# Kernel optimization log

Hardware: AMD Instinct MI355X
Metric: run time of the kernel (lower is better)

The kernel has to match this reference:

```python
import jax, jax.numpy as jnp
import numpy as np

REG_LAMBDA = 1e-4
NEG_SLOPE = 0.2
EPS = 1e-12


def _aggregate(edge_row, edge_col, edge_val, user_emb, item_emb, W_gcn, b_gcn, W_bi, b_bi):
    num_users = user_emb.shape[0]
    N = num_users + item_emb.shape[0]
    ego = jnp.concatenate([user_emb, item_emb], axis=0)  # [N, D]
    all_embs = [ego]
    n_layers = W_gcn.shape[0]
    for l in range(n_layers):
        # sparse adjacency spmm: side = A @ ego
        side = jax.ops.segment_sum(edge_val[:, None] * ego[edge_col], edge_row, num_segments=N)
        sum_e = side @ W_gcn[l] + b_gcn[l]
        bi_e = (ego * side) @ W_bi[l] + b_bi[l]
        ego = jax.nn.leaky_relu(sum_e + bi_e, negative_slope=NEG_SLOPE)
        # mess_dropout disabled (eval-mode); L2-normalize rows
        norm = jnp.maximum(jnp.linalg.norm(ego, axis=1, keepdims=True), EPS)
        all_embs.append(ego / norm)
    final = jnp.concatenate(all_embs, axis=1)  # [N, (L+1)*D]
    return final[:num_users], final[num_users:]


def reference(user, positive, negative, edge_row, edge_col, edge_val,
              user_emb, item_emb, W_gcn, b_gcn, W_bi, b_bi):
    users_all, items_all = _aggregate(edge_row, edge_col, edge_val,
                                      user_emb, item_emb, W_gcn, b_gcn, W_bi, b_bi)
    u = users_all[user]
    p = items_all[positive]
    n = items_all[negative]
    pos_score = jnp.sum(u * p, axis=1)
    neg_score = jnp.sum(u * n, axis=1)
    # BPR: -mean(log sigmoid(pos - neg)) == mean(softplus(neg - pos))
    bpr_loss = jnp.mean(jax.nn.softplus(neg_score - pos_score))
    ego_pos = item_emb[positive]
    ego_neg = item_emb[negative]
    B = user.shape[0]
    reg_loss = REG_LAMBDA * 0.5 * (jnp.sum(ego_pos ** 2) + jnp.sum(ego_neg ** 2)) / B
    return jnp.stack([bpr_loss, reg_loss])


def setup_inputs() -> dict:
    key = jax.random.key(0)
    ks = jax.random.split(key, 12)
    U, I, D, L, NNZ, B = 50000, 100000, 128, 3, 4800000, 4096
    N = U + I
    xav = (6.0 / (D + D)) ** 0.5
    return {
        "user": jax.random.randint(ks[0], (B,), 0, U, dtype=jnp.int32),
        "positive": jax.random.randint(ks[1], (B,), 0, I, dtype=jnp.int32),
        "negative": jax.random.randint(ks[2], (B,), 0, I, dtype=jnp.int32),
        "edge_row": jax.random.randint(ks[3], (NNZ,), 0, N, dtype=jnp.int32),
        "edge_col": jax.random.randint(ks[4], (NNZ,), 0, N, dtype=jnp.int32),
        "edge_val": jax.random.uniform(ks[5], (NNZ,), dtype=jnp.float32) / 32.0,
        "user_emb": jax.random.normal(ks[6], (U, D), dtype=jnp.float32) * 0.1,
        "item_emb": jax.random.normal(ks[7], (I, D), dtype=jnp.float32) * 0.1,
        "W_gcn": jax.random.uniform(ks[8], (L, D, D), minval=-xav, maxval=xav, dtype=jnp.float32),
        "b_gcn": jax.random.uniform(ks[9], (L, D), minval=-xav, maxval=xav, dtype=jnp.float32),
        "W_bi": jax.random.uniform(ks[10], (L, D, D), minval=-xav, maxval=xav, dtype=jnp.float32),
        "b_bi": jax.random.uniform(ks[11], (L, D), minval=-xav, maxval=xav, dtype=jnp.float32),
    }
```

## Files before the change

kernel.cpp:

```cpp
#include <hip/hip_runtime.h>
#include <math.h>

#define D 128
#define NEG_SLOPE 0.2f
#define REG_LAMBDA 1e-4f
#define NORM_EPS 1e-12f

#define RPB 256
#define RPB_SHIFT 8
#define MAXB 1024
#define CHUNK 4096
#define TCSH 14
#define KEYMAX 4096

#define XPAD 264

using bf16x8 = __attribute__((ext_vector_type(8))) short;
using f32x4  = __attribute__((ext_vector_type(4))) float;
using f32x2  = __attribute__((ext_vector_type(2))) float;

__device__ __forceinline__ float wave_red(float v){
  #pragma unroll
  for (int o = 32; o > 0; o >>= 1) v += __shfl_xor(v, o, 64);
  return v;
}

__device__ __forceinline__ unsigned short f2bf(float f){
  unsigned int u = __float_as_uint(f);
  unsigned int r = (u + 0x7fffu + ((u >> 16) & 1u)) >> 16;
  return (unsigned short)r;
}
__device__ __forceinline__ float bf_lo(unsigned int x){ return __uint_as_float(x << 16); }
__device__ __forceinline__ float bf_hi(unsigned int x){ return __uint_as_float(x & 0xffff0000u); }

__global__ __launch_bounds__(256) void toq_kernel(const float* __restrict__ src, unsigned int* __restrict__ dstb,
                                                  unsigned short* __restrict__ dst8, int npairs){
  int i = blockIdx.x*256 + threadIdx.x;
  if (i >= npairs) return;
  float2 v = ((const float2*)src)[i];
  dstb[i] = (unsigned int)f2bf(v.x) | ((unsigned int)f2bf(v.y) << 16);
  int p = __builtin_amdgcn_cvt_pk_fp8_f32(v.x, v.y, 0, false);
  dst8[i] = (unsigned short)(p & 0xffff);
}

__global__ __launch_bounds__(256) void wconv_kernel(const float* __restrict__ Wg, const float* __restrict__ Wb,
                                                    unsigned short* __restrict__ Wf, int L){
  int idx = blockIdx.x*256 + threadIdx.x;
  int total = L * 256 * D;
  if (idx >= total) return;
  int l = idx >> 15;
  int rem = idx & 32767;
  int k = rem >> 7;
  int n = rem & 127;
  float v = (k < 128) ? Wg[((size_t)l*128 + k)*D + n] : Wb[((size_t)l*128 + (k-128))*D + n];
  int ks = k >> 5, quad = (k >> 3) & 3, j = k & 7;
  int t = n >> 4, ln = (quad << 4) | (n & 15);
  Wf[(size_t)l*32768 + (((ks*8 + t)*64 + ln)*8 + j)] = f2bf(v);
}

__global__ __launch_bounds__(256) void bhist_kernel(const int* __restrict__ erow, int* __restrict__ bcnt, int nnz, int nbk){
  __shared__ int h[MAXB];
  for (int i = threadIdx.x; i < nbk; i += 256) h[i] = 0;
  __syncthreads();
  int stride = gridDim.x * 256;
  for (int e = blockIdx.x*256 + threadIdx.x; e < nnz; e += stride)
    atomicAdd(&h[erow[e] >> RPB_SHIFT], 1);
  __syncthreads();
  for (int i = threadIdx.x; i < nbk; i += 256){
    int c = h[i];
    if (c) atomicAdd(&bcnt[i], c);
  }
}

__global__ __launch_bounds__(1024) void bscan_kernel(const int* __restrict__ bcnt, int* __restrict__ bbase,
                                                     int* __restrict__ bcur, int* __restrict__ rowptr,
                                                     int nbk, int nnz, int n){
  __shared__ int tmp[1024];
  int t = threadIdx.x;
  int v = (t < nbk) ? bcnt[t] : 0;
  tmp[t] = v; __syncthreads();
  #pragma unroll
  for (int off = 1; off < 1024; off <<= 1){
    int a = (t >= off) ? tmp[t-off] : 0; __syncthreads();
    tmp[t] += a; __syncthreads();
  }
  if (t < nbk){ int b = tmp[t] - v; bbase[t] = b; bcur[t] = b; }
  if (t == 0){ bbase[nbk] = nnz; rowptr[n] = nnz; }
}

__global__ __launch_bounds__(256) void bscatter_kernel(const int* __restrict__ erow, const int* __restrict__ ecol,
                                                       const float* __restrict__ eval, int* __restrict__ bcur,
                                                       int2* __restrict__ ebuf, int nnz, int nbk){
  __shared__ int2 ls[CHUNK];
  __shared__ int gdst[CHUNK];
  __shared__ int h[MAXB];
  __shared__ int hx[MAXB];
  __shared__ int tmp[256];
  int tid = threadIdx.x;
  int base = blockIdx.x * CHUNK;
  int cn = min(CHUNK, nnz - base);
  for (int i = tid; i < nbk; i += 256) h[i] = 0;
  __syncthreads();
  for (int i = tid; i < cn; i += 256)
    atomicAdd(&h[erow[base+i] >> RPB_SHIFT], 1);
  __syncthreads();
  int b0 = tid*4;
  int c0=0,c1=0,c2=0,c3=0;
  if (b0 < nbk){
    c0 = h[b0];
    if (b0+1 < nbk) c1 = h[b0+1];
    if (b0+2 < nbk) c2 = h[b0+2];
    if (b0+3 < nbk) c3 = h[b0+3];
  }
  int tsum = c0+c1+c2+c3;
  tmp[tid] = tsum; __syncthreads();
  #pragma unroll
  for (int off = 1; off < 256; off <<= 1){
    int a = (tid >= off) ? tmp[tid-off] : 0; __syncthreads();
    tmp[tid] += a; __syncthreads();
  }
  int tbase = tmp[tid] - tsum;
  if (b0 < nbk){
    hx[b0] = tbase;
    if (b0+1 < nbk) hx[b0+1] = tbase + c0;
    if (b0+2 < nbk) hx[b0+2] = tbase + c0 + c1;
    if (b0+3 < nbk) hx[b0+3] = tbase + c0 + c1 + c2;
  }
  __syncthreads();
  for (int i = tid; i < nbk; i += 256){
    int c = h[i];
    if (c > 0){
      int gb = atomicAdd(&bcur[i], c);
      h[i] = gb - hx[i];
    }
  }
  __syncthreads();
  for (int i = tid; i < cn; i += 256){
    int r = erow[base+i];
    int b = r >> RPB_SHIFT;
    int x = ecol[base+i] | ((r & (RPB-1)) << 20);
    int lpos = atomicAdd(&hx[b], 1);
    ls[lpos] = make_int2(x, __float_as_int(eval[base+i]));
    gdst[lpos] = h[b] + lpos;
  }
  __syncthreads();
  for (int i = tid; i < cn; i += 256)
    ebuf[gdst[i]] = ls[i];
}

__global__ __launch_bounds__(256) void fscatter_kernel(const int2* __restrict__ ebuf, const int* __restrict__ bbase,
                                                       int2* __restrict__ ep, int* __restrict__ rowptr,
                                                       int Tc, int n){
  __shared__ int h[KEYMAX];
  __shared__ int tsum[256];
  int b = blockIdx.x;
  int tid = threadIdx.x;
  int s = bbase[b], e = bbase[b+1];
  int row0 = b << RPB_SHIFT;
  int nk = 256 * Tc;
  for (int i = tid; i < nk; i += 256) h[i] = 0;
  __syncthreads();
  for (int i = s + tid; i < e; i += 256){
    int x = ebuf[i].x;
    int key = ((x >> 20) & 255) * Tc + ((x & 0xFFFFF) >> TCSH);
    atomicAdd(&h[key], 1);
  }
  __syncthreads();
  int my0 = tid * Tc;
  int run = 0;
  for (int j = 0; j < Tc; j++){
    int c = h[my0 + j]; h[my0 + j] = run; run += c;
  }
  tsum[tid] = run; __syncthreads();
  #pragma unroll
  for (int off = 1; off < 256; off <<= 1){
    int a = (tid >= off) ? tsum[tid-off] : 0; __syncthreads();
    tsum[tid] += a; __syncthreads();
  }
  int bt = tsum[tid] - run;
  for (int j = 0; j < Tc; j++) h[my0 + j] += bt;
  __syncthreads();
  if (row0 + tid < n) rowptr[row0 + tid] = s + h[my0];
  __syncthreads();
  for (int i = s + tid; i < e; i += 256){
    int2 E = ebuf[i];
    int x = E.x;
    int col = x & 0xFFFFF;
    int key = ((x >> 20) & 255) * Tc + (col >> TCSH);
    int p = atomicAdd(&h[key], 1);
    ep[s + p] = make_int2(col << 7, E.y);
  }
}

__global__ __launch_bounds__(256) void spmm_kernel(const int* __restrict__ rowptr, const int2* __restrict__ ep,
                                                   const unsigned char* __restrict__ egof8,
                                                   unsigned int* __restrict__ sideb, int n){
  int w = (blockIdx.x*256 + threadIdx.x) >> 6;
  int lane = threadIdx.x & 63;
  if (w >= n) return;
  int s = rowptr[w], e = rowptr[w+1];
  int sub  = lane >> 4;
  int half = lane & 15;
  float acc[8];
  #pragma unroll
  for (int j = 0; j < 8; j++) acc[j] = 0.f;
  for (int base = s; base < e; base += 16){
    int2 E[4]; uint2 X[4];
    #pragma unroll
    for (int k = 0; k < 4; k++){
      int idx = base + 4*k + sub;
      idx = idx < e ? idx : e - 1;
      E[k] = ep[idx];
    }
    #pragma unroll
    for (int k = 0; k < 4; k++)
      X[k] = *(const uint2*)(egof8 + (size_t)(unsigned)E[k].x + half*8);
    #pragma unroll
    for (int k = 0; k < 4; k++){
      float v = (base + 4*k + sub < e) ? __int_as_float(E[k].y) : 0.f;
      f32x2 d0 = __builtin_amdgcn_cvt_pk_f32_fp8((int)X[k].x, false);
      f32x2 d1 = __builtin_amdgcn_cvt_pk_f32_fp8((int)X[k].x, true);
      f32x2 d2 = __builtin_amdgcn_cvt_pk_f32_fp8((int)X[k].y, false);
      f32x2 d3 = __builtin_amdgcn_cvt_pk_f32_fp8((int)X[k].y, true);
      acc[0] = fmaf(v, d0[0], acc[0]); acc[1] = fmaf(v, d0[1], acc[1]);
      acc[2] = fmaf(v, d1[0], acc[2]); acc[3] = fmaf(v, d1[1], acc[3]);
      acc[4] = fmaf(v, d2[0], acc[4]); acc[5] = fmaf(v, d2[1], acc[5]);
      acc[6] = fmaf(v, d3[0], acc[6]); acc[7] = fmaf(v, d3[1], acc[7]);
    }
  }
  #pragma unroll
  for (int j = 0; j < 8; j++){
    acc[j] += __shfl_xor(acc[j], 16, 64);
    acc[j] += __shfl_xor(acc[j], 32, 64);
  }
  if (lane < 16){
    unsigned int o0 = (unsigned int)f2bf(acc[0]) | ((unsigned int)f2bf(acc[1]) << 16);
    unsigned int o1 = (unsigned int)f2bf(acc[2]) | ((unsigned int)f2bf(acc[3]) << 16);
    unsigned int o2 = (unsigned int)f2bf(acc[4]) | ((unsigned int)f2bf(acc[5]) << 16);
    unsigned int o3 = (unsigned int)f2bf(acc[6]) | ((unsigned int)f2bf(acc[7]) << 16);
    *(uint4*)(sideb + (size_t)w*64 + half*4) = make_uint4(o0, o1, o2, o3);
  }
}

__global__ __launch_bounds__(256, 4) void transform_kernel(const unsigned int* __restrict__ sideb,
                                                           unsigned int* __restrict__ egob,
                                                           unsigned char* __restrict__ egof8,
                                                           const unsigned short* __restrict__ Wf,
                                                           const float* __restrict__ b1, const float* __restrict__ b2,
                                                           int n){
  __shared__ __align__(16) unsigned short X[64 * XPAD];
  int row0 = blockIdx.x * 64;
  int tid = threadIdx.x;
  for (int idx = tid; idx < 64*64; idx += 256){
    int r = idx >> 6, cp = idx & 63;
    int row = row0 + r;
    unsigned int sv = 0, pv = 0;
    if (row < n){
      unsigned int s2 = sideb[(size_t)row*64 + cp];
      unsigned int eb = egob[(size_t)row*64 + cp];
      sv = s2;
      pv = (unsigned int)f2bf(bf_lo(s2) * bf_lo(eb)) | ((unsigned int)f2bf(bf_hi(s2) * bf_hi(eb)) << 16);
    }
    *(unsigned int*)&X[r*XPAD + 2*cp]       = sv;
    *(unsigned int*)&X[r*XPAD + 128 + 2*cp] = pv;
  }
  __syncthreads();

  int wave = tid >> 6, lane = tid & 63;
  int wr0 = wave * 16;
  int m = lane & 15, quad = lane >> 4;

  f32x4 acc[8];
  #pragma unroll
  for (int t = 0; t < 8; t++) acc[t] = (f32x4){0.f, 0.f, 0.f, 0.f};

  const unsigned short* arow = &X[(wr0 + m)*XPAD + quad*8];
  #pragma unroll
  for (int ks = 0; ks < 8; ks++){
    bf16x8 a = *(const bf16x8*)(arow + ks*32);
    #pragma unroll
    for (int t = 0; t < 8; t++){
      bf16x8 b = *(const bf16x8*)&Wf[((ks*8 + t)*64 + lane)*8];
      acc[t] = __builtin_amdgcn_mfma_f32_16x16x32_bf16(a, b, acc[t], 0, 0, 0);
    }
  }

  unsigned short* ego16 = (unsigned short*)egob;
  #pragma unroll
  for (int t = 0; t < 8; t++){
    int col = t*16 + m;
    float bb = b1[col] + b2[col];
    #pragma unroll
    for (int r = 0; r < 4; r++){
      int row = row0 + wr0 + quad*4 + r;
      if (row < n){
        float v = acc[t][r] + bb;
        v = v > 0.f ? v : NEG_SLOPE*v;
        ego16[(size_t)row*D + col] = f2bf(v);
        egof8[(size_t)row*D + col] =
            (unsigned char)(__builtin_amdgcn_cvt_pk_fp8_f32(v, v, 0, false) & 0xff);
      }
    }
  }
}

__global__ __launch_bounds__(256) void score_kernel(const unsigned int* __restrict__ egob, const int* __restrict__ user,
                                                    const int* __restrict__ pos, const int* __restrict__ neg,
                                                    float* __restrict__ pacc, float* __restrict__ nacc,
                                                    int B, int U, int normalize){
  int w = (blockIdx.x*256 + threadIdx.x) >> 6;
  int lane = threadIdx.x & 63;
  if (w >= B) return;
  size_t ur = (size_t)user[w] * 64;
  size_t pr = ((size_t)U + pos[w]) * 64;
  size_t nr = ((size_t)U + neg[w]) * 64;
  unsigned int ub = egob[ur + lane], pb = egob[pr + lane], nb = egob[nr + lane];
  float ux = bf_lo(ub), uy = bf_hi(ub);
  float px = bf_lo(pb), py = bf_hi(pb);
  float nx = bf_lo(nb), ny = bf_hi(nb);
  float dup = ux*px + uy*py;
  float dun = ux*nx + uy*ny;
  float nu  = ux*ux + uy*uy;
  float np  = px*px + py*py;
  float nn  = nx*nx + ny*ny;
  dup = wave_red(dup); dun = wave_red(dun);
  nu = wave_red(nu); np = wave_red(np); nn = wave_red(nn);
  if (lane == 0){
    if (normalize){
      float inu = 1.f / fmaxf(sqrtf(nu), NORM_EPS);
      float inp = 1.f / fmaxf(sqrtf(np), NORM_EPS);
      float inn = 1.f / fmaxf(sqrtf(nn), NORM_EPS);
      pacc[w] += dup * inu * inp;
      nacc[w] += dun * inu * inn;
    } else {
      pacc[w] += dup;
      nacc[w] += dun;
    }
  }
}

__global__ __launch_bounds__(256) void reg_kernel(const float* __restrict__ item, const int* __restrict__ pos,
                                                  const int* __restrict__ neg, float* __restrict__ reg_out, int B){
  int w = (blockIdx.x*256 + threadIdx.x) >> 6;
  int lane = threadIdx.x & 63;
  if (w >= B) return;
  const float2* it = (const float2*)item;
  float2 pv = it[(size_t)pos[w]*64 + lane];
  float2 nv = it[(size_t)neg[w]*64 + lane];
  float v = pv.x*pv.x + pv.y*pv.y + nv.x*nv.x + nv.y*nv.y;
  v = wave_red(v);
  if (lane == 0) atomicAdd(reg_out, v);
}

__global__ __launch_bounds__(256) void final_kernel(const float* __restrict__ pacc, const float* __restrict__ nacc,
                                                    const float* __restrict__ reg_sum, float* __restrict__ out, int B){
  __shared__ float red[256];
  float s = 0.f;
  for (int i = threadIdx.x; i < B; i += 256){
    float x = nacc[i] - pacc[i];
    s += (x > 0.f) ? x + log1pf(expf(-x)) : log1pf(expf(x));
  }
  red[threadIdx.x] = s; __syncthreads();
  for (int o = 128; o > 0; o >>= 1){
    if (threadIdx.x < o) red[threadIdx.x] += red[threadIdx.x + o];
    __syncthreads();
  }
  if (threadIdx.x == 0){
    out[0] = red[0] / (float)B;
    out[1] = REG_LAMBDA * 0.5f * reg_sum[0] / (float)B;
  }
}

extern "C" void kernel_launch(void* const* d_in, const int* in_sizes, int n_in,
                              void* d_out, int out_size, void* d_ws, size_t ws_size,
                              hipStream_t stream) {
  const int*   user = (const int*)d_in[0];
  const int*   pos  = (const int*)d_in[1];
  const int*   neg  = (const int*)d_in[2];
  const int*   erow = (const int*)d_in[3];
  const int*   ecol = (const int*)d_in[4];
  const float* eval = (const float*)d_in[5];
  const float* uemb = (const float*)d_in[6];
  const float* iemb = (const float*)d_in[7];
  const float* Wg   = (const float*)d_in[8];
  const float* bg   = (const float*)d_in[9];
  const float* Wb   = (const float*)d_in[10];
  const float* bb   = (const float*)d_in[11];

  int B   = in_sizes[0];
  int NNZ = in_sizes[3];
  int U   = in_sizes[6] / D;
  int I   = in_sizes[7] / D;
  int N   = U + I;
  int L   = in_sizes[9] / D;
  int nbk = (N + RPB - 1) >> RPB_SHIFT;
  int Tc  = (N + (1 << TCSH) - 1) >> TCSH;

  char* wsp = (char*)d_ws;
  auto alloc = [&](size_t bytes) -> char* {
    char* p = wsp; wsp += (bytes + 255) & ~(size_t)255; return p;
  };
  size_t side_bytes = (size_t)N * D * 2;
  size_t ebuf_bytes = (size_t)NNZ * 8;
  unsigned int*  sideb  = (unsigned int*)alloc(side_bytes > ebuf_bytes ? side_bytes : ebuf_bytes);
  unsigned int*  egob   = (unsigned int*)alloc((size_t)N * D * 2);
  unsigned short* egof8 = (unsigned short*)alloc((size_t)N * D);
  int2*          ep     = (int2*) alloc((size_t)NNZ * 8);
  unsigned short* Wf    = (unsigned short*)alloc((size_t)L * 256 * D * 2);
  int*           rowptr = (int*)  alloc((size_t)(N + 1) * 4);
  int*           bcnt   = (int*)  alloc((size_t)MAXB * 4);
  int*           bbase  = (int*)  alloc((size_t)(MAXB + 1) * 4);
  int*           bcur   = (int*)  alloc((size_t)MAXB * 4);
  float*         pacc   = (float*)alloc((size_t)B * 4);
  float*         nacc   = (float*)alloc((size_t)B * 4);
  float*         regs   = (float*)alloc(256);
  int2*          ebuf   = (int2*)sideb;

  hipMemsetAsync(bcnt, 0, (size_t)nbk * 4, stream);
  hipMemsetAsync(pacc, 0, (size_t)B * 4, stream);
  hipMemsetAsync(nacc, 0, (size_t)B * 4, stream);
  hipMemsetAsync(regs, 0, 4, stream);

  toq_kernel<<<(U*64 + 255) / 256, 256, 0, stream>>>(uemb, egob, egof8, U*64);
  toq_kernel<<<(I*64 + 255) / 256, 256, 0, stream>>>(iemb, egob + (size_t)U*64, egof8 + (size_t)U*64, I*64);
  wconv_kernel<<<(L*256*D + 255) / 256, 256, 0, stream>>>(Wg, Wb, Wf, L);

  bhist_kernel<<<2048, 256, 0, stream>>>(erow, bcnt, NNZ, nbk);
  bscan_kernel<<<1, 1024, 0, stream>>>(bcnt, bbase, bcur, rowptr, nbk, NNZ, N);
  bscatter_kernel<<<(NNZ + CHUNK - 1) / CHUNK, 256, 0, stream>>>(erow, ecol, eval, bcur, ebuf, NNZ, nbk);
  fscatter_kernel<<<nbk, 256, 0, stream>>>(ebuf, bbase, ep, rowptr, Tc, N);

  score_kernel<<<(B + 3) / 4, 256, 0, stream>>>(egob, user, pos, neg, pacc, nacc, B, U, 0);

  for (int l = 0; l < L; l++){
    spmm_kernel<<<(N + 3) / 4, 256, 0, stream>>>(rowptr, ep, (const unsigned char*)egof8, sideb, N);
    transform_kernel<<<(N + 63) / 64, 256, 0, stream>>>(
        sideb, egob, (unsigned char*)egof8, Wf + (size_t)l * 256 * D,
        bg + (size_t)l * D, bb + (size_t)l * D, N);
    score_kernel<<<(B + 3) / 4, 256, 0, stream>>>(egob, user, pos, neg, pacc, nacc, B, U, 1);
  }

  reg_kernel<<<(B + 3) / 4, 256, 0, stream>>>(iemb, pos, neg, regs, B);
  final_kernel<<<1, 256, 0, stream>>>(pacc, nacc, regs, (float*)d_out, B);
}
```

Measured before the change: 909.6 us.

## Fuse SpMM into dense transform kernel with ping-pong fp8 buffers

Merges the per-row SpMM gather and the MFMA layer transform into one kernel. Each wave aggregates 16 rows straight into shared memory, including the bf16 side*ego product, so the side buffer no longer makes a global round trip. The fp8 ego copy now alternates between two buffers so gathers never read rows being overwritten. It also adds packed FMA, a split between full and tail edge chunks, and raised wave priority around the MFMA loop. In exchange each block runs its rows in sequence before the GEMM, which lowers parallelism during the latency-bound gather phase.

```diff
diff --git a/kernel.cpp b/kernel.cpp
--- a/kernel.cpp
+++ b/kernel.cpp
@@ -32,6 +32,13 @@
 }
 __device__ __forceinline__ float bf_lo(unsigned int x){ return __uint_as_float(x << 16); }
 __device__ __forceinline__ float bf_hi(unsigned int x){ return __uint_as_float(x & 0xffff0000u); }
+__device__ __forceinline__ float bf_rnd(float x){ return __uint_as_float(((unsigned int)f2bf(x)) << 16); }
+
+__device__ __forceinline__ f32x2 pk_fma(f32x2 a, f32x2 b, f32x2 c){
+  f32x2 d;
+  asm("v_pk_fma_f32 %0, %1, %2, %3" : "=v"(d) : "v"(a), "v"(b), "v"(c));
+  return d;
+}
 
 __global__ __launch_bounds__(256) void toq_kernel(const float* __restrict__ src, unsigned int* __restrict__ dstb,
                                                   unsigned short* __restrict__ dst8, int npairs){
@@ -192,89 +199,113 @@
   }
 }
 
-__global__ __launch_bounds__(256) void spmm_kernel(const int* __restrict__ rowptr, const int2* __restrict__ ep,
-                                                   const unsigned char* __restrict__ egof8,
-                                                   unsigned int* __restrict__ sideb, int n){
-  int w = (blockIdx.x*256 + threadIdx.x) >> 6;
-  int lane = threadIdx.x & 63;
-  if (w >= n) return;
-  int s = rowptr[w], e = rowptr[w+1];
+__global__ __launch_bounds__(256, 4) void sptrans_kernel(const int* __restrict__ rowptr, const int2* __restrict__ ep,
+                                                         const unsigned char* __restrict__ f8in,
+                                                         unsigned int* __restrict__ egob,
+                                                         unsigned char* __restrict__ f8out,
+                                                         const unsigned short* __restrict__ Wf,
+                                                         const float* __restrict__ b1, const float* __restrict__ b2,
+                                                         int n){
+  __shared__ __align__(16) unsigned short X[64 * XPAD];
+  int tid  = threadIdx.x;
+  int row0 = blockIdx.x * 64;
+  int wave = tid >> 6, lane = tid & 63;
   int sub  = lane >> 4;
   int half = lane & 15;
-  float acc[8];
-  #pragma unroll
-  for (int j = 0; j < 8; j++) acc[j] = 0.f;
-  for (int base = s; base < e; base += 16){
-    int2 E[4]; uint2 X[4];
+  const unsigned char* f8h = f8in + half*8;
+
+  int rowA = row0 + wave*16;
+  int sCur = (rowA < n) ? rowptr[rowA] : 0;
+
+  #pragma unroll 1
+  for (int i = 0; i < 16; ++i){
+    int r   = wave*16 + i;
+    int row = rowA + i;
+    int s = sCur;
+    int e = (row < n) ? rowptr[row+1] : s;
+    sCur = e;
+
+    f32x2 acc2[4];
     #pragma unroll
-    for (int k = 0; k < 4; k++){
-      int idx = base + 4*k + sub;
-      idx = idx < e ? idx : e - 1;
-      E[k] = ep[idx];
+    for (int j = 0; j < 4; j++) acc2[j] = (f32x2){0.f, 0.f};
+
+    int nfull = (e - s) >> 4;
+    const int2* pe = ep + s;
+    for (int f = 0; f < nfull; ++f, pe += 16){
+      int2 E[4]; uint2 Xv[4];
+      #pragma unroll
+      for (int k = 0; k < 4; k++) E[k] = pe[4*k + sub];
+      #pragma unroll
+      for (int k = 0; k < 4; k++)
+        Xv[k] = *(const uint2*)(f8h + (size_t)(unsigned)E[k].x);
+      #pragma unroll
+      for (int k = 0; k < 4; k++){
+        float v = __int_as_float(E[k].y);
+        f32x2 vv = (f32x2){v, v};
+        acc2[0] = pk_fma(vv, __builtin_amdgcn_cvt_pk_f32_fp8((int)Xv[k].x, false), acc2[0]);
+        acc2[1] = pk_fma(vv, __builtin_amdgcn_cvt_pk_f32_fp8((int)Xv[k].x, true ), acc2[1]);
+        acc2[2] = pk_fma(vv, __builtin_amdgcn_cvt_pk_f32_fp8((int)Xv[k].y, false), acc2[2]);
+        acc2[3] = pk_fma(vv, __builtin_amdgcn_cvt_pk_f32_fp8((int)Xv[k].y, true ), acc2[3]);
+      }
+    }
+    int base = s + (nfull << 4);
+    if (base < e){
+      int2 E[4]; uint2 Xv[4];
+      #pragma unroll
+      for (int k = 0; k < 4; k++){
+        int idx = base + 4*k + sub;
+        idx = idx < e ? idx : e - 1;
+        E[k] = ep[idx];
+      }
+      #pragma unroll
+      for (int k = 0; k < 4; k++)
+        Xv[k] = *(const uint2*)(f8h + (size_t)(unsigned)E[k].x);
+      #pragma unroll
+      for (int k = 0; k < 4; k++){
+        float v = (base + 4*k + sub < e) ? __int_as_float(E[k].y) : 0.f;
+        f32x2 vv = (f32x2){v, v};
+        acc2[0] = pk_fma(vv, __builtin_amdgcn_cvt_pk_f32_fp8((int)Xv[k].x, false), acc2[0]);
+        acc2[1] = pk_fma(vv, __builtin_amdgcn_cvt_pk_f32_fp8((int)Xv[k].x, true ), acc2[1]);
+        acc2[2] = pk_fma(vv, __builtin_amdgcn_cvt_pk_f32_fp8((int)Xv[k].y, false), acc2[2]);
+        acc2[3] = pk_fma(vv, __builtin_amdgcn_cvt_pk_f32_fp8((int)Xv[k].y, true ), acc2[3]);
+      }
     }
     #pragma unroll
-    for (int k = 0; k < 4; k++)
-      X[k] = *(const uint2*)(egof8 + (size_t)(unsigned)E[k].x + half*8);
-    #pragma unroll
-    for (int k = 0; k < 4; k++){
-      float v = (base + 4*k + sub < e) ? __int_as_float(E[k].y) : 0.f;
-      f32x2 d0 = __builtin_amdgcn_cvt_pk_f32_fp8((int)X[k].x, false);
-      f32x2 d1 = __builtin_amdgcn_cvt_pk_f32_fp8((int)X[k].x, true);
-      f32x2 d2 = __builtin_amdgcn_cvt_pk_f32_fp8((int)X[k].y, false);
-      f32x2 d3 = __builtin_amdgcn_cvt_pk_f32_fp8((int)X[k].y, true);
-      acc[0] = fmaf(v, d0[0], acc[0]); acc[1] = fmaf(v, d0[1], acc[1]);
-      acc[2] = fmaf(v, d1[0], acc[2]); acc[3] = fmaf(v, d1[1], acc[3]);
-      acc[4] = fmaf(v, d2[0], acc[4]); acc[5] = fmaf(v, d2[1], acc[5]);
-      acc[6] = fmaf(v, d3[0], acc[6]); acc[7] = fmaf(v, d3[1], acc[7]);
-    }
-  }
-  #pragma unroll
-  for (int j = 0; j < 8; j++){
-    acc[j] += __shfl_xor(acc[j], 16, 64);
-    acc[j] += __shfl_xor(acc[j], 32, 64);
-  }
-  if (lane < 16){
-    unsigned int o0 = (unsigned int)f2bf(acc[0]) | ((unsigned int)f2bf(acc[1]) << 16);
-    unsigned int o1 = (unsigned int)f2bf(acc[2]) | ((unsigned int)f2bf(acc[3]) << 16);
-    unsigned int o2 = (unsigned int)f2bf(acc[4]) | ((unsigned int)f2bf(acc[5]) << 16);
-    unsigned int o3 = (unsigned int)f2bf(acc[6]) | ((unsigned int)f2bf(acc[7]) << 16);
-    *(uint4*)(sideb + (size_t)w*64 + half*4) = make_uint4(o0, o1, o2, o3);
-  }
-}
-
-__global__ __launch_bounds__(256, 4) void transform_kernel(const unsigned int* __restrict__ sideb,
-                                                           unsigned int* __restrict__ egob,
-                                                           unsigned char* __restrict__ egof8,
-                                                           const unsigned short* __restrict__ Wf,
-                                                           const float* __restrict__ b1, const float* __restrict__ b2,
-                                                           int n){
-  __shared__ __align__(16) unsigned short X[64 * XPAD];
-  int row0 = blockIdx.x * 64;
-  int tid = threadIdx.x;
-  for (int idx = tid; idx < 64*64; idx += 256){
-    int r = idx >> 6, cp = idx & 63;
-    int row = row0 + r;
-    unsigned int sv = 0, pv = 0;
-    if (row < n){
-      unsigned int s2 = sideb[(size_t)row*64 + cp];
-      unsigned int eb = egob[(size_t)row*64 + cp];
-      sv = s2;
-      pv = (unsigned int)f2bf(bf_lo(s2) * bf_lo(eb)) | ((unsigned int)f2bf(bf_hi(s2) * bf_hi(eb)) << 16);
-    }
-    *(unsigned int*)&X[r*XPAD + 2*cp]       = sv;
-    *(unsigned int*)&X[r*XPAD + 128 + 2*cp] = pv;
-  }
-  __syncthreads();
-
-  int wave = tid >> 6, lane = tid & 63;
+    for (int j = 0; j < 4; j++){
+      acc2[j][0] += __shfl_xor(acc2[j][0], 16, 64);
+      acc2[j][1] += __shfl_xor(acc2[j][1], 16, 64);
+      acc2[j][0] += __shfl_xor(acc2[j][0], 32, 64);
+      acc2[j][1] += __shfl_xor(acc2[j][1], 32, 64);
+    }
+    if (sub == 0){
+      unsigned int o0 = (unsigned int)f2bf(acc2[0][0]) | ((unsigned int)f2bf(acc2[0][1]) << 16);
+      unsigned int o1 = (unsigned int)f2bf(acc2[1][0]) | ((unsigned int)f2bf(acc2[1][1]) << 16);
+      unsigned int o2 = (unsigned int)f2bf(acc2[2][0]) | ((unsigned int)f2bf(acc2[2][1]) << 16);
+      unsigned int o3 = (unsigned int)f2bf(acc2[3][0]) | ((unsigned int)f2bf(acc2[3][1]) << 16);
+      *(uint4*)&X[r*XPAD + 8*half] = make_uint4(o0, o1, o2, o3);
+    } else if (sub < 3){
+      int u = (sub - 1) << 1;
+      uint2 eg = make_uint2(0u, 0u);
+      if (row < n) eg = *(const uint2*)(egob + (size_t)row*64 + 4*half + u);
+      f32x2 aL = acc2[u], aH = acc2[u+1];
+      unsigned int p0 = (unsigned int)f2bf(bf_rnd(aL[0]) * bf_lo(eg.x)) |
+                        ((unsigned int)f2bf(bf_rnd(aL[1]) * bf_hi(eg.x)) << 16);
+      unsigned int p1 = (unsigned int)f2bf(bf_rnd(aH[0]) * bf_lo(eg.y)) |
+                        ((unsigned int)f2bf(bf_rnd(aH[1]) * bf_hi(eg.y)) << 16);
+      *(uint2*)&X[r*XPAD + 128 + 8*half + (u << 1)] = make_uint2(p0, p1);
+    }
+  }
+  __syncthreads();
+
   int wr0 = wave * 16;
-  int m = lane & 15, quad = lane >> 4;
+  int m = half, quad = sub;
 
   f32x4 acc[8];
   #pragma unroll
   for (int t = 0; t < 8; t++) acc[t] = (f32x4){0.f, 0.f, 0.f, 0.f};
 
   const unsigned short* arow = &X[(wr0 + m)*XPAD + quad*8];
+  __builtin_amdgcn_s_setprio(1);
   #pragma unroll
   for (int ks = 0; ks < 8; ks++){
     bf16x8 a = *(const bf16x8*)(arow + ks*32);
@@ -284,6 +315,7 @@
       acc[t] = __builtin_amdgcn_mfma_f32_16x16x32_bf16(a, b, acc[t], 0, 0, 0);
     }
   }
+  __builtin_amdgcn_s_setprio(0);
 
   unsigned short* ego16 = (unsigned short*)egob;
   #pragma unroll
@@ -291,13 +323,13 @@
     int col = t*16 + m;
     float bb = b1[col] + b2[col];
     #pragma unroll
-    for (int r = 0; r < 4; r++){
-      int row = row0 + wr0 + quad*4 + r;
+    for (int rr = 0; rr < 4; rr++){
+      int row = row0 + wr0 + quad*4 + rr;
       if (row < n){
-        float v = acc[t][r] + bb;
+        float v = acc[t][rr] + bb;
         v = v > 0.f ? v : NEG_SLOPE*v;
         ego16[(size_t)row*D + col] = f2bf(v);
-        egof8[(size_t)row*D + col] =
+        f8out[(size_t)row*D + col] =
             (unsigned char)(__builtin_amdgcn_cvt_pk_fp8_f32(v, v, 0, false) & 0xff);
       }
     }
@@ -402,7 +434,7 @@
   };
   size_t side_bytes = (size_t)N * D * 2;
   size_t ebuf_bytes = (size_t)NNZ * 8;
-  unsigned int*  sideb  = (unsigned int*)alloc(side_bytes > ebuf_bytes ? side_bytes : ebuf_bytes);
+  unsigned int*  slot0  = (unsigned int*)alloc(side_bytes > ebuf_bytes ? side_bytes : ebuf_bytes);
   unsigned int*  egob   = (unsigned int*)alloc((size_t)N * D * 2);
   unsigned short* egof8 = (unsigned short*)alloc((size_t)N * D);
   int2*          ep     = (int2*) alloc((size_t)NNZ * 8);
@@ -414,7 +446,9 @@
   float*         pacc   = (float*)alloc((size_t)B * 4);
   float*         nacc   = (float*)alloc((size_t)B * 4);
   float*         regs   = (float*)alloc(256);
-  int2*          ebuf   = (int2*)sideb;
+  int2*          ebuf   = (int2*)slot0;
+  unsigned char* f8A    = (unsigned char*)egof8;
+  unsigned char* f8B    = (unsigned char*)slot0;
 
   hipMemsetAsync(bcnt, 0, (size_t)nbk * 4, stream);
   hipMemsetAsync(pacc, 0, (size_t)B * 4, stream);
@@ -433,9 +467,10 @@
   score_kernel<<<(B + 3) / 4, 256, 0, stream>>>(egob, user, pos, neg, pacc, nacc, B, U, 0);
 
   for (int l = 0; l < L; l++){
-    spmm_kernel<<<(N + 3) / 4, 256, 0, stream>>>(rowptr, ep, (const unsigned char*)egof8, sideb, N);
-    transform_kernel<<<(N + 63) / 64, 256, 0, stream>>>(
-        sideb, egob, (unsigned char*)egof8, Wf + (size_t)l * 256 * D,
+    const unsigned char* fin  = (l & 1) ? f8B : f8A;
+    unsigned char*       fout = (l & 1) ? f8A : f8B;
+    sptrans_kernel<<<(N + 63) / 64, 256, 0, stream>>>(
+        rowptr, ep, fin, egob, fout, Wf + (size_t)l * 256 * D,
         bg + (size_t)l * D, bb + (size_t)l * D, N);
     score_kernel<<<(B + 3) / 4, 256, 0, stream>>>(egob, user, pos, neg, pacc, nacc, B, U, 1);
   }
```

After: 1.047 ms. 15.1% more time.
